# Kernel tuning notes

Measured on AMD Instinct MI355X. Metric: run time of the kernel, lower is better.

The kernel has to match this reference:

```python
import jax, jax.numpy as jnp
import numpy as np

N = 100_000      # total nodes in batched graph
E = 1_600_000    # directed edges (avg degree 16)
G = 64           # graphs in batch
F_IN = 64        # num_features
H = 64           # hl1
GF = 32          # num_global_feats
GH = 32          # global_hl1 (hard-coded in module)


def setup_inputs() -> dict:
    key = jax.random.key(0)
    ks = jax.random.split(key, 24)
    s = 0.1  # weight scale
    inp = {
        "x": jax.random.normal(ks[0], (N, F_IN), jnp.float32),
        "global_feats": jax.random.normal(ks[1], (G * GF,), jnp.float32),
        "conv0_w": jax.random.normal(ks[2], (F_IN, H), jnp.float32) * s,
        "conv0_b": jax.random.normal(ks[3], (H,), jnp.float32) * s,
        "conv1_w": jax.random.normal(ks[4], (H, H), jnp.float32) * s,
        "conv1_b": jax.random.normal(ks[5], (H,), jnp.float32) * s,
        "conv2_w": jax.random.normal(ks[6], (H, H), jnp.float32) * s,
        "conv2_b": jax.random.normal(ks[7], (H,), jnp.float32) * s,
        "lin1_w": jax.random.normal(ks[8], (H, H), jnp.float32) * s,
        "lin1_b": jax.random.normal(ks[9], (H,), jnp.float32) * s,
        "glob_w": jax.random.normal(ks[10], (GF, GH), jnp.float32) * s,
        "glob_b": jax.random.normal(ks[11], (GH,), jnp.float32) * s,
        "lin2_w": jax.random.normal(ks[12], (H + GH, H), jnp.float32) * s,
        "lin2_b": jax.random.normal(ks[13], (H,), jnp.float32) * s,
        "lin3_w": jax.random.normal(ks[14], (H, H), jnp.float32) * s,
        "lin3_b": jax.random.normal(ks[15], (H,), jnp.float32) * s,
        "lin4_w": jax.random.normal(ks[16], (H, 1), jnp.float32) * s,
        "lin4_b": jax.random.normal(ks[17], (1,), jnp.float32) * s,
        "edge_index": jax.random.randint(ks[18], (2, E), 0, N, jnp.int64) if jax.config.jax_enable_x64 else jax.random.randint(ks[18], (2, E), 0, N, jnp.int32),
        "node_graph_ids": jnp.sort(jax.random.randint(ks[19], (N,), 0, G, jnp.int32)),
    }
    return inp


def reference(x, global_feats, conv0_w, conv0_b, conv1_w, conv1_b, conv2_w, conv2_b,
              lin1_w, lin1_b, glob_w, glob_b, lin2_w, lin2_b, lin3_w, lin3_b,
              lin4_w, lin4_b, edge_index, node_graph_ids):
    # --- GCN symmetric normalization with self-loops (PyG GCNConv default) ---
    loops = jnp.arange(N, dtype=edge_index.dtype)
    src = jnp.concatenate([edge_index[0], loops])  # [E+N]
    dst = jnp.concatenate([edge_index[1], loops])
    deg = jax.ops.segment_sum(jnp.ones_like(dst, jnp.float32), dst, num_segments=N)
    dis = jax.lax.rsqrt(deg)  # deg >= 1 thanks to self-loops
    norm = (dis[src] * dis[dst])[:, None]  # [E+N, 1]

    def gcn_conv(h, W, b):
        h = h @ W                                    # [N, H]
        msg = h[src] * norm                          # gather + scale  [E+N, H]
        return jax.ops.segment_sum(msg, dst, num_segments=N) + b  # scatter-add

    h = jax.nn.relu(gcn_conv(x, conv0_w, conv0_b))
    h = jax.nn.relu(gcn_conv(h, conv1_w, conv1_b))
    h = jax.nn.relu(gcn_conv(h, conv2_w, conv2_b))

    # --- per-graph sum pooling (contiguous slices == segment_sum on sorted ids) ---
    pooled = jax.ops.segment_sum(h, node_graph_ids, num_segments=G)  # [G, H]

    gx = jax.nn.relu(global_feats.reshape(G, GF) @ glob_w + glob_b)  # [G, GH]

    z = jax.nn.relu(pooled @ lin1_w + lin1_b)
    z = jnp.concatenate([z, gx], axis=1)             # [G, H+GH]
    z = jax.nn.relu(z @ lin2_w + lin2_b)
    z = jax.nn.relu(z @ lin3_w + lin3_b)
    out = (z @ lin4_w + lin4_b).squeeze(1)           # [G]
    return out
```

## Files before the change

kernel.cpp:

```cpp
#include <hip/hip_runtime.h>
#include <hip/hip_bf16.h>

#define NTHREADS 256
#define CAP 6144
#define P1_EDGES 8192

typedef unsigned int uint32;

__device__ __forceinline__ void fma8(float4& A0, float4& A1, uint4 v, float w) {
    A0.x += __uint_as_float(v.x << 16) * w;
    A0.y += __uint_as_float(v.x & 0xffff0000u) * w;
    A0.z += __uint_as_float(v.y << 16) * w;
    A0.w += __uint_as_float(v.y & 0xffff0000u) * w;
    A1.x += __uint_as_float(v.z << 16) * w;
    A1.y += __uint_as_float(v.z & 0xffff0000u) * w;
    A1.z += __uint_as_float(v.w << 16) * w;
    A1.w += __uint_as_float(v.w & 0xffff0000u) * w;
}
__device__ __forceinline__ void acc8(float4& A0, float4& A1, uint4 v) {
    A0.x += __uint_as_float(v.x << 16);
    A0.y += __uint_as_float(v.x & 0xffff0000u);
    A0.z += __uint_as_float(v.y << 16);
    A0.w += __uint_as_float(v.y & 0xffff0000u);
    A1.x += __uint_as_float(v.z << 16);
    A1.y += __uint_as_float(v.z & 0xffff0000u);
    A1.z += __uint_as_float(v.w << 16);
    A1.w += __uint_as_float(v.w & 0xffff0000u);
}

__device__ __forceinline__ void stage_W(const float* __restrict__ W, uint32* sWp) {
    int t = threadIdx.x;
#pragma unroll
    for (int i = 0; i < 8; i++) {
        int idx = t + NTHREADS * i;
        int p = idx >> 6, c = idx & 63;
        ushort lo = __bfloat16_as_ushort(__float2bfloat16(W[(2 * p) * 64 + c]));
        ushort hi = __bfloat16_as_ushort(__float2bfloat16(W[(2 * p + 1) * 64 + c]));
        sWp[idx] = (uint32)lo | ((uint32)hi << 16);
    }
}

__device__ __forceinline__ void gemm_compute(
    const uint32* __restrict__ sWp, const float* __restrict__ sX,
    const float* __restrict__ sD, __hip_bfloat16* __restrict__ out,
    int n_rows, int row_base) {
    int t = threadIdx.x;
    int c = t & 63;
    int r0 = t >> 6;
    float acc[16];
#pragma unroll
    for (int j = 0; j < 16; j++) acc[j] = 0.f;

    for (int k = 0; k < 64; k += 4) {
        uint32 u01 = sWp[((k >> 1) + 0) * 64 + c];
        uint32 u23 = sWp[((k >> 1) + 1) * 64 + c];
        float w0 = __uint_as_float(u01 << 16);
        float w1 = __uint_as_float(u01 & 0xffff0000u);
        float w2 = __uint_as_float(u23 << 16);
        float w3 = __uint_as_float(u23 & 0xffff0000u);
#pragma unroll
        for (int j = 0; j < 16; j++) {
            float4 xv = *(const float4*)(sX + (r0 + 4 * j) * 64 + k);
            acc[j] += xv.x * w0 + xv.y * w1 + xv.z * w2 + xv.w * w3;
        }
    }

#pragma unroll
    for (int j = 0; j < 16; j++) {
        int r = row_base + r0 + 4 * j;
        if (r < n_rows) {
            float s = sD ? sD[r0 + 4 * j] : 1.0f;
            out[(size_t)r * 64 + c] = __float2bfloat16(s * acc[j]);
        }
    }
}

__global__ __launch_bounds__(NTHREADS) void pass1_gemm0(
    const int* __restrict__ ei, int nE, int* gcur, uint32* __restrict__ pbuf, int npart,
    const float* __restrict__ x, __hip_bfloat16* __restrict__ U,
    const float* __restrict__ W, int n_rows, int nP1) {
    __shared__ __align__(16) uint32 sWp[32 * 64];
    __shared__ __align__(16) float sX[64 * 64];

    int bid = blockIdx.x;
    int t = threadIdx.x;

    if (bid < nP1) {
        int* hist = (int*)sX;
        int* base = hist + npart;
        int* cnt  = base + npart;
        for (int i = t; i < npart; i += NTHREADS) { hist[i] = 0; cnt[i] = 0; }
        __syncthreads();

        int e0 = bid * P1_EDGES;
#pragma unroll 4
        for (int j = 0; j < P1_EDGES / NTHREADS; j++) {
            int e = e0 + j * NTHREADS + t;
            if (e < nE) atomicAdd(&hist[ei[nE + e] >> 8], 1);
        }
        __syncthreads();
        for (int i = t; i < npart; i += NTHREADS) {
            base[i] = hist[i] ? atomicAdd(&gcur[i * 16], hist[i]) : 0;
        }
        __syncthreads();
#pragma unroll 4
        for (int j = 0; j < P1_EDGES / NTHREADS; j++) {
            int e = e0 + j * NTHREADS + t;
            if (e < nE) {
                int s = ei[e];
                int d = ei[nE + e];
                int p = d >> 8;
                int off = atomicAdd(&cnt[p], 1);
                int pos = base[p] + off;
                if (pos < CAP) pbuf[(size_t)p * CAP + pos] = ((uint32)s << 8) | (uint32)(d & 255);
            }
        }
        return;
    }

    int row_base = (bid - nP1) * 64;
    stage_W(W, sWp);
    float4* sX4 = (float4*)sX;
#pragma unroll
    for (int i = 0; i < 4; i++) {
        int idx = t + NTHREADS * i;
        int r = row_base + (idx >> 4);
        float4 v = make_float4(0.f, 0.f, 0.f, 0.f);
        if (r < n_rows) v = ((const float4*)(x + (size_t)r * 64))[idx & 15];
        sX4[idx] = v;
    }
    __syncthreads();
    gemm_compute(sWp, sX, nullptr, U, n_rows, row_base);
}

__global__ __launch_bounds__(512) void scanP(const int* __restrict__ gcur, int* pbase,
                                             int npart, int n, int nE, int* row_ptr) {
    __shared__ int sm[512];
    int t = threadIdx.x;
    int v = (t < npart) ? gcur[t * 16] : 0;
    sm[t] = v;
    __syncthreads();
    for (int off = 1; off < 512; off <<= 1) {
        int a = (t >= off) ? sm[t - off] : 0;
        __syncthreads();
        sm[t] += a;
        __syncthreads();
    }
    if (t < npart) pbase[t] = sm[t] - v;
    if (t == 0) row_ptr[n] = nE;
}

__global__ __launch_bounds__(NTHREADS) void pass2(
    const uint32* __restrict__ pbuf, const int* __restrict__ gcur,
    const int* __restrict__ pbase, int* __restrict__ row_ptr,
    float* __restrict__ dis, int* __restrict__ col, int n) {
    __shared__ int hist[256];
    __shared__ int excl[256];
    __shared__ int cnt[256];
    __shared__ int sm[256];

    int p = blockIdx.x;
    int t = threadIdx.x;
    hist[t] = 0;
    cnt[t] = 0;
    __syncthreads();

    int total = gcur[p * 16];
    if (total > CAP) total = CAP;
    const uint32* pb = pbuf + (size_t)p * CAP;

    for (int i = t; i < total; i += NTHREADS) atomicAdd(&hist[pb[i] & 255], 1);
    __syncthreads();

    sm[t] = hist[t];
    __syncthreads();
    for (int off = 1; off < 256; off <<= 1) {
        int a = (t >= off) ? sm[t - off] : 0;
        __syncthreads();
        sm[t] += a;
        __syncthreads();
    }
    excl[t] = sm[t] - hist[t];
    __syncthreads();

    int rbase = pbase[p];
    int node = p * 256 + t;
    if (node < n) {
        row_ptr[node] = rbase + excl[t];
        dis[node] = rsqrtf(1.0f + (float)hist[t]);
    }

    for (int i = t; i < total; i += NTHREADS) {
        uint32 v = pb[i];
        int dl = v & 255;
        int off = atomicAdd(&cnt[dl], 1);
        col[rbase + excl[dl] + off] = (int)(v >> 8);
    }
}

template <bool WEIGHTED>
__device__ __forceinline__ void gather_row(
    const uint4* __restrict__ T8, const float* __restrict__ dis,
    const float* __restrict__ bias,
    const int* __restrict__ row_ptr, const int* __restrict__ col,
    int node, int q, float* __restrict__ sXrow, int n) {
    float4 o0, o1;
    if (node < n) {
        float dn = dis[node];
        float4 a0 = make_float4(0.f, 0.f, 0.f, 0.f);
        float4 a1 = make_float4(0.f, 0.f, 0.f, 0.f);
        {
            uint4 sv = T8[(size_t)node * 8 + q];
            if (WEIGHTED) fma8(a0, a1, sv, dn);
            else          acc8(a0, a1, sv);
        }
        int e0 = row_ptr[node];
        int e1 = row_ptr[node + 1];
        int e = e0;
        for (; e + 7 < e1; e += 8) {
            int s0 = col[e],     s1 = col[e + 1], s2 = col[e + 2], s3 = col[e + 3];
            int s4 = col[e + 4], s5 = col[e + 5], s6 = col[e + 6], s7 = col[e + 7];
            uint4 v0 = T8[(size_t)s0 * 8 + q];
            uint4 v1 = T8[(size_t)s1 * 8 + q];
            uint4 v2 = T8[(size_t)s2 * 8 + q];
            uint4 v3 = T8[(size_t)s3 * 8 + q];
            uint4 v4 = T8[(size_t)s4 * 8 + q];
            uint4 v5 = T8[(size_t)s5 * 8 + q];
            uint4 v6 = T8[(size_t)s6 * 8 + q];
            uint4 v7 = T8[(size_t)s7 * 8 + q];
            if (WEIGHTED) {
                fma8(a0, a1, v0, dis[s0]); fma8(a0, a1, v1, dis[s1]);
                fma8(a0, a1, v2, dis[s2]); fma8(a0, a1, v3, dis[s3]);
                fma8(a0, a1, v4, dis[s4]); fma8(a0, a1, v5, dis[s5]);
                fma8(a0, a1, v6, dis[s6]); fma8(a0, a1, v7, dis[s7]);
            } else {
                acc8(a0, a1, v0); acc8(a0, a1, v1); acc8(a0, a1, v2); acc8(a0, a1, v3);
                acc8(a0, a1, v4); acc8(a0, a1, v5); acc8(a0, a1, v6); acc8(a0, a1, v7);
            }
        }
        for (; e + 3 < e1; e += 4) {
            int s0 = col[e], s1 = col[e + 1], s2 = col[e + 2], s3 = col[e + 3];
            uint4 v0 = T8[(size_t)s0 * 8 + q];
            uint4 v1 = T8[(size_t)s1 * 8 + q];
            uint4 v2 = T8[(size_t)s2 * 8 + q];
            uint4 v3 = T8[(size_t)s3 * 8 + q];
            if (WEIGHTED) {
                fma8(a0, a1, v0, dis[s0]); fma8(a0, a1, v1, dis[s1]);
                fma8(a0, a1, v2, dis[s2]); fma8(a0, a1, v3, dis[s3]);
            } else {
                acc8(a0, a1, v0); acc8(a0, a1, v1); acc8(a0, a1, v2); acc8(a0, a1, v3);
            }
        }
        for (; e < e1; e++) {
            int s0 = col[e];
            uint4 v0 = T8[(size_t)s0 * 8 + q];
            if (WEIGHTED) fma8(a0, a1, v0, dis[s0]);
            else          acc8(a0, a1, v0);
        }
        float4 b0 = ((const float4*)bias)[q * 2];
        float4 b1 = ((const float4*)bias)[q * 2 + 1];
        o0.x = fmaxf(b0.x + dn * a0.x, 0.f);
        o0.y = fmaxf(b0.y + dn * a0.y, 0.f);
        o0.z = fmaxf(b0.z + dn * a0.z, 0.f);
        o0.w = fmaxf(b0.w + dn * a0.w, 0.f);
        o1.x = fmaxf(b1.x + dn * a1.x, 0.f);
        o1.y = fmaxf(b1.y + dn * a1.y, 0.f);
        o1.z = fmaxf(b1.z + dn * a1.z, 0.f);
        o1.w = fmaxf(b1.w + dn * a1.w, 0.f);
    } else {
        o0 = make_float4(0.f, 0.f, 0.f, 0.f);
        o1 = o0;
    }
    ((float4*)sXrow)[q * 2] = o0;
    ((float4*)sXrow)[q * 2 + 1] = o1;
}

template <bool WEIGHTED>
__global__ __launch_bounds__(NTHREADS) void agg_gemm(
    const __hip_bfloat16* __restrict__ Tin, __hip_bfloat16* __restrict__ Tout,
    const float* __restrict__ W, const float* __restrict__ dis,
    const float* __restrict__ bias,
    const int* __restrict__ row_ptr, const int* __restrict__ col, int n) {
    __shared__ __align__(16) uint32 sWp[32 * 64];
    __shared__ __align__(16) float sX[64 * 64];
    __shared__ float sD[64];
    int t = threadIdx.x;
    int row_base = blockIdx.x * 64;

    stage_W(W, sWp);
    if (t < 64) {
        int r = row_base + t;
        sD[t] = (r < n) ? dis[r] : 0.f;
    }

    const uint4* T8 = (const uint4*)Tin;
    int q = t & 7;
    int l = t >> 3;
    gather_row<WEIGHTED>(T8, dis, bias, row_ptr, col, row_base + l,      q, sX + l * 64,        n);
    gather_row<WEIGHTED>(T8, dis, bias, row_ptr, col, row_base + 32 + l, q, sX + (32 + l) * 64, n);
    __syncthreads();

    gemm_compute(sWp, sX, sD, Tout, n, row_base);
}

__global__ __launch_bounds__(NTHREADS) void agg_pool(
    const __hip_bfloat16* __restrict__ Tin,
    const float* __restrict__ dis, const float* __restrict__ bias,
    const int* __restrict__ row_ptr, const int* __restrict__ col,
    const int* __restrict__ gid, float* __restrict__ pooled, int n) {
    __shared__ __align__(16) float sX[64 * 64];
    __shared__ int sG[64];
    int t = threadIdx.x;
    int row_base = blockIdx.x * 64;

    if (t < 64) {
        int r = row_base + t;
        sG[t] = (r < n) ? gid[r] : -1;
    }

    const uint4* T8 = (const uint4*)Tin;
    int q = t & 7;
    int l = t >> 3;
    gather_row<false>(T8, dis, bias, row_ptr, col, row_base + l,      q, sX + l * 64,        n);
    gather_row<false>(T8, dis, bias, row_ptr, col, row_base + 32 + l, q, sX + (32 + l) * 64, n);
    __syncthreads();

    int f = t & 63;
    int w = t >> 6;
    float racc = 0.f;
    int cur = -1;
#pragma unroll
    for (int i = 0; i < 16; i++) {
        int r = i * 4 + w;
        int g = sG[r];
        if (g != cur) {
            if (cur >= 0 && racc != 0.f) atomicAdd(&pooled[cur * 64 + f], racc);
            racc = 0.f;
            cur = g;
        }
        if (g >= 0) racc += sX[r * 64 + f];
    }
    if (cur >= 0 && racc != 0.f) atomicAdd(&pooled[cur * 64 + f], racc);
}

__global__ __launch_bounds__(NTHREADS) void head_kernel(
    const float* __restrict__ pooled, const float* __restrict__ gf,
    const float* __restrict__ glob_w, const float* __restrict__ glob_b,
    const float* __restrict__ lin1_w, const float* __restrict__ lin1_b,
    const float* __restrict__ lin2_w, const float* __restrict__ lin2_b,
    const float* __restrict__ lin3_w, const float* __restrict__ lin3_b,
    const float* __restrict__ lin4_w, const float* __restrict__ lin4_b,
    float* __restrict__ out) {
    __shared__ float gx[64 * 32];
    __shared__ float zA[64 * 64];
    __shared__ float zB[64 * 64];
    int t = threadIdx.x;

    for (int i = t; i < 64 * 32; i += NTHREADS) {
        int g = i >> 5, j = i & 31;
        float acc = glob_b[j];
        for (int k = 0; k < 32; k++) acc += gf[g * 32 + k] * glob_w[k * 32 + j];
        gx[i] = fmaxf(acc, 0.f);
    }
    for (int i = t; i < 4096; i += NTHREADS) {
        int g = i >> 6, j = i & 63;
        float acc = lin1_b[j];
        for (int k = 0; k < 64; k++) acc += pooled[g * 64 + k] * lin1_w[k * 64 + j];
        zA[i] = fmaxf(acc, 0.f);
    }
    __syncthreads();
    for (int i = t; i < 4096; i += NTHREADS) {
        int g = i >> 6, j = i & 63;
        float acc = lin2_b[j];
        for (int k = 0; k < 64; k++) acc += zA[g * 64 + k] * lin2_w[k * 64 + j];
        for (int k = 0; k < 32; k++) acc += gx[g * 32 + k] * lin2_w[(64 + k) * 64 + j];
        zB[i] = fmaxf(acc, 0.f);
    }
    __syncthreads();
    for (int i = t; i < 4096; i += NTHREADS) {
        int g = i >> 6, j = i & 63;
        float acc = lin3_b[j];
        for (int k = 0; k < 64; k++) acc += zB[g * 64 + k] * lin3_w[k * 64 + j];
        zA[i] = fmaxf(acc, 0.f);
    }
    __syncthreads();
    if (t < 64) {
        float acc = lin4_b[0];
        for (int k = 0; k < 64; k++) acc += zA[t * 64 + k] * lin4_w[k];
        out[t] = acc;
    }
}

extern "C" void kernel_launch(void* const* d_in, const int* in_sizes, int n_in,
                              void* d_out, int out_size, void* d_ws, size_t ws_size,
                              hipStream_t stream) {
    const float* x      = (const float*)d_in[0];
    const float* gf     = (const float*)d_in[1];
    const float* conv_w[3] = {(const float*)d_in[2], (const float*)d_in[4], (const float*)d_in[6]};
    const float* conv_b[3] = {(const float*)d_in[3], (const float*)d_in[5], (const float*)d_in[7]};
    const float* lin1_w = (const float*)d_in[8];
    const float* lin1_b = (const float*)d_in[9];
    const float* glob_w = (const float*)d_in[10];
    const float* glob_b = (const float*)d_in[11];
    const float* lin2_w = (const float*)d_in[12];
    const float* lin2_b = (const float*)d_in[13];
    const float* lin3_w = (const float*)d_in[14];
    const float* lin3_b = (const float*)d_in[15];
    const float* lin4_w = (const float*)d_in[16];
    const float* lin4_b = (const float*)d_in[17];
    const int* ei  = (const int*)d_in[18];
    const int* gid = (const int*)d_in[19];

    const int N = in_sizes[0] / 64;
    const int E = in_sizes[18] / 2;
    const int NPART = (N + 255) >> 8;

    char* ws = (char*)d_ws;
    float* dis     = (float*)ws;                 ws += (size_t)N * 4;
    float* pooled  = (float*)ws;                 ws += 4096 * 4;
    __hip_bfloat16* U  = (__hip_bfloat16*)ws;    ws += (size_t)N * 64 * 2;
    __hip_bfloat16* T1 = (__hip_bfloat16*)ws;    ws += (size_t)N * 64 * 2;
    int*   row_ptr = (int*)ws;                   ws += ((size_t)N + 4) * 4;
    int*   col     = (int*)ws;                   ws += (size_t)E * 4;
    uint32* pbuf   = (uint32*)ws;                ws += (size_t)NPART * CAP * 4;
    int*   gcur    = (int*)ws;                   ws += (size_t)NPART * 16 * 4;
    int*   pbase   = (int*)ws;                   ws += (size_t)((NPART + 15) & ~15) * 4;

    const int nP1 = (E + P1_EDGES - 1) / P1_EDGES;
    const int gemm_blocks = (N + 63) / 64;

    hipMemsetAsync(gcur, 0, (size_t)NPART * 16 * 4, stream);
    hipMemsetAsync(pooled, 0, 4096 * 4, stream);
    pass1_gemm0<<<nP1 + gemm_blocks, NTHREADS, 0, stream>>>(
        ei, E, gcur, pbuf, NPART, x, U, conv_w[0], N, nP1);

    scanP<<<1, 512, 0, stream>>>(gcur, pbase, NPART, N, E, row_ptr);
    pass2<<<NPART, NTHREADS, 0, stream>>>(pbuf, gcur, pbase, row_ptr, dis, col, N);

    agg_gemm<true><<<gemm_blocks, NTHREADS, 0, stream>>>(
        U, T1, conv_w[1], dis, conv_b[0], row_ptr, col, N);

    agg_gemm<false><<<gemm_blocks, NTHREADS, 0, stream>>>(
        T1, U, conv_w[2], dis, conv_b[1], row_ptr, col, N);

    agg_pool<<<gemm_blocks, NTHREADS, 0, stream>>>(
        U, dis, conv_b[2], row_ptr, col, gid, pooled, N);

    head_kernel<<<1, NTHREADS, 0, stream>>>(pooled, gf,
                                            glob_w, glob_b, lin1_w, lin1_b,
                                            lin2_w, lin2_b, lin3_w, lin3_b,
                                            lin4_w, lin4_b, (float*)d_out);
}
```

Measured before the change: 254.7 us.

## Split bf16 feature tables into two 32-column planes for gather locality

Node feature tables are stored as two separate planes of 32 bf16 columns each instead of one 64-column row. Gathers read one plane for all edges, then the other, with 4 threads per row instead of 8, so each plane's working set is half the size and may stay in cache better. The weights are also kept in shared memory as fp32 instead of packed bf16, which removes the unpacking in the GEMM inner loop but doubles the LDS footprint. The trade-off is reading the col/dis indices twice per node and a different occupancy profile.

Measured after the change: 281.2 us. 10.4% more time.

```diff
diff --git a/kernel.cpp b/kernel.cpp
--- a/kernel.cpp
+++ b/kernel.cpp
@@ -28,21 +28,18 @@
     A1.w += __uint_as_float(v.w & 0xffff0000u);
 }
 
-__device__ __forceinline__ void stage_W(const float* __restrict__ W, uint32* sWp) {
-    int t = threadIdx.x;
-#pragma unroll
-    for (int i = 0; i < 8; i++) {
-        int idx = t + NTHREADS * i;
-        int p = idx >> 6, c = idx & 63;
-        ushort lo = __bfloat16_as_ushort(__float2bfloat16(W[(2 * p) * 64 + c]));
-        ushort hi = __bfloat16_as_ushort(__float2bfloat16(W[(2 * p + 1) * 64 + c]));
-        sWp[idx] = (uint32)lo | ((uint32)hi << 16);
-    }
+__device__ __forceinline__ void stage_W(const float* __restrict__ W, float* sW) {
+    int t = threadIdx.x;
+    const float4* W4 = (const float4*)W;
+    float4* sW4 = (float4*)sW;
+#pragma unroll
+    for (int i = 0; i < 4; i++) sW4[t + NTHREADS * i] = W4[t + NTHREADS * i];
 }
 
 __device__ __forceinline__ void gemm_compute(
-    const uint32* __restrict__ sWp, const float* __restrict__ sX,
-    const float* __restrict__ sD, __hip_bfloat16* __restrict__ out,
+    const float* __restrict__ sW, const float* __restrict__ sX,
+    const float* __restrict__ sD,
+    __hip_bfloat16* __restrict__ out_lo, __hip_bfloat16* __restrict__ out_hi,
     int n_rows, int row_base) {
     int t = threadIdx.x;
     int c = t & 63;
@@ -52,12 +49,10 @@
     for (int j = 0; j < 16; j++) acc[j] = 0.f;
 
     for (int k = 0; k < 64; k += 4) {
-        uint32 u01 = sWp[((k >> 1) + 0) * 64 + c];
-        uint32 u23 = sWp[((k >> 1) + 1) * 64 + c];
-        float w0 = __uint_as_float(u01 << 16);
-        float w1 = __uint_as_float(u01 & 0xffff0000u);
-        float w2 = __uint_as_float(u23 << 16);
-        float w3 = __uint_as_float(u23 & 0xffff0000u);
+        float w0 = sW[(k + 0) * 64 + c];
+        float w1 = sW[(k + 1) * 64 + c];
+        float w2 = sW[(k + 2) * 64 + c];
+        float w3 = sW[(k + 3) * 64 + c];
 #pragma unroll
         for (int j = 0; j < 16; j++) {
             float4 xv = *(const float4*)(sX + (r0 + 4 * j) * 64 + k);
@@ -65,21 +60,24 @@
         }
     }
 
+    __hip_bfloat16* outp = (c < 32) ? out_lo : out_hi;
+    int cl = c & 31;
 #pragma unroll
     for (int j = 0; j < 16; j++) {
         int r = row_base + r0 + 4 * j;
         if (r < n_rows) {
             float s = sD ? sD[r0 + 4 * j] : 1.0f;
-            out[(size_t)r * 64 + c] = __float2bfloat16(s * acc[j]);
+            outp[(size_t)r * 32 + cl] = __float2bfloat16(s * acc[j]);
         }
     }
 }
 
 __global__ __launch_bounds__(NTHREADS) void pass1_gemm0(
     const int* __restrict__ ei, int nE, int* gcur, uint32* __restrict__ pbuf, int npart,
-    const float* __restrict__ x, __hip_bfloat16* __restrict__ U,
+    const float* __restrict__ x,
+    __hip_bfloat16* __restrict__ U_lo, __hip_bfloat16* __restrict__ U_hi,
     const float* __restrict__ W, int n_rows, int nP1) {
-    __shared__ __align__(16) uint32 sWp[32 * 64];
+    __shared__ __align__(16) float sW[64 * 64];
     __shared__ __align__(16) float sX[64 * 64];
 
     int bid = blockIdx.x;
@@ -119,7 +117,7 @@
     }
 
     int row_base = (bid - nP1) * 64;
-    stage_W(W, sWp);
+    stage_W(W, sW);
     float4* sX4 = (float4*)sX;
 #pragma unroll
     for (int i = 0; i < 4; i++) {
@@ -130,7 +128,7 @@
         sX4[idx] = v;
     }
     __syncthreads();
-    gemm_compute(sWp, sX, nullptr, U, n_rows, row_base);
+    gemm_compute(sW, sX, nullptr, U_lo, U_hi, n_rows, row_base);
 }
 
 __global__ __launch_bounds__(512) void scanP(const int* __restrict__ gcur, int* pbase,
@@ -199,9 +197,9 @@
 }
 
 template <bool WEIGHTED>
-__device__ __forceinline__ void gather_row(
-    const uint4* __restrict__ T8, const float* __restrict__ dis,
-    const float* __restrict__ bias,
+__device__ __forceinline__ void gather_plane(
+    const uint4* __restrict__ P, const float* __restrict__ dis,
+    const float* __restrict__ biasp,
     const int* __restrict__ row_ptr, const int* __restrict__ col,
     int node, int q, float* __restrict__ sXrow, int n) {
     float4 o0, o1;
@@ -210,7 +208,7 @@
         float4 a0 = make_float4(0.f, 0.f, 0.f, 0.f);
         float4 a1 = make_float4(0.f, 0.f, 0.f, 0.f);
         {
-            uint4 sv = T8[(size_t)node * 8 + q];
+            uint4 sv = P[(size_t)node * 4 + q];
             if (WEIGHTED) fma8(a0, a1, sv, dn);
             else          acc8(a0, a1, sv);
         }
@@ -220,14 +218,14 @@
         for (; e + 7 < e1; e += 8) {
             int s0 = col[e],     s1 = col[e + 1], s2 = col[e + 2], s3 = col[e + 3];
             int s4 = col[e + 4], s5 = col[e + 5], s6 = col[e + 6], s7 = col[e + 7];
-            uint4 v0 = T8[(size_t)s0 * 8 + q];
-            uint4 v1 = T8[(size_t)s1 * 8 + q];
-            uint4 v2 = T8[(size_t)s2 * 8 + q];
-            uint4 v3 = T8[(size_t)s3 * 8 + q];
-            uint4 v4 = T8[(size_t)s4 * 8 + q];
-            uint4 v5 = T8[(size_t)s5 * 8 + q];
-            uint4 v6 = T8[(size_t)s6 * 8 + q];
-            uint4 v7 = T8[(size_t)s7 * 8 + q];
+            uint4 v0 = P[(size_t)s0 * 4 + q];
+            uint4 v1 = P[(size_t)s1 * 4 + q];
+            uint4 v2 = P[(size_t)s2 * 4 + q];
+            uint4 v3 = P[(size_t)s3 * 4 + q];
+            uint4 v4 = P[(size_t)s4 * 4 + q];
+            uint4 v5 = P[(size_t)s5 * 4 + q];
+            uint4 v6 = P[(size_t)s6 * 4 + q];
+            uint4 v7 = P[(size_t)s7 * 4 + q];
             if (WEIGHTED) {
                 fma8(a0, a1, v0, dis[s0]); fma8(a0, a1, v1, dis[s1]);
                 fma8(a0, a1, v2, dis[s2]); fma8(a0, a1, v3, dis[s3]);
@@ -240,10 +238,10 @@
         }
         for (; e + 3 < e1; e += 4) {
             int s0 = col[e], s1 = col[e + 1], s2 = col[e + 2], s3 = col[e + 3];
-            uint4 v0 = T8[(size_t)s0 * 8 + q];
-            uint4 v1 = T8[(size_t)s1 * 8 + q];
-            uint4 v2 = T8[(size_t)s2 * 8 + q];
-            uint4 v3 = T8[(size_t)s3 * 8 + q];
+            uint4 v0 = P[(size_t)s0 * 4 + q];
+            uint4 v1 = P[(size_t)s1 * 4 + q];
+            uint4 v2 = P[(size_t)s2 * 4 + q];
+            uint4 v3 = P[(size_t)s3 * 4 + q];
             if (WEIGHTED) {
                 fma8(a0, a1, v0, dis[s0]); fma8(a0, a1, v1, dis[s1]);
                 fma8(a0, a1, v2, dis[s2]); fma8(a0, a1, v3, dis[s3]);
@@ -253,12 +251,12 @@
         }
         for (; e < e1; e++) {
             int s0 = col[e];
-            uint4 v0 = T8[(size_t)s0 * 8 + q];
+            uint4 v0 = P[(size_t)s0 * 4 + q];
             if (WEIGHTED) fma8(a0, a1, v0, dis[s0]);
             else          acc8(a0, a1, v0);
         }
-        float4 b0 = ((const float4*)bias)[q * 2];
-        float4 b1 = ((const float4*)bias)[q * 2 + 1];
+        float4 b0 = ((const float4*)biasp)[q * 2];
+        float4 b1 = ((const float4*)biasp)[q * 2 + 1];
         o0.x = fmaxf(b0.x + dn * a0.x, 0.f);
         o0.y = fmaxf(b0.y + dn * a0.y, 0.f);
         o0.z = fmaxf(b0.z + dn * a0.z, 0.f);
@@ -277,34 +275,36 @@
 
 template <bool WEIGHTED>
 __global__ __launch_bounds__(NTHREADS) void agg_gemm(
-    const __hip_bfloat16* __restrict__ Tin, __hip_bfloat16* __restrict__ Tout,
+    const __hip_bfloat16* __restrict__ Tin_lo, const __hip_bfloat16* __restrict__ Tin_hi,
+    __hip_bfloat16* __restrict__ Tout_lo, __hip_bfloat16* __restrict__ Tout_hi,
     const float* __restrict__ W, const float* __restrict__ dis,
     const float* __restrict__ bias,
     const int* __restrict__ row_ptr, const int* __restrict__ col, int n) {
-    __shared__ __align__(16) uint32 sWp[32 * 64];
+    __shared__ __align__(16) float sW[64 * 64];
     __shared__ __align__(16) float sX[64 * 64];
     __shared__ float sD[64];
     int t = threadIdx.x;
     int row_base = blockIdx.x * 64;
 
-    stage_W(W, sWp);
+    stage_W(W, sW);
     if (t < 64) {
         int r = row_base + t;
         sD[t] = (r < n) ? dis[r] : 0.f;
     }
 
-    const uint4* T8 = (const uint4*)Tin;
-    int q = t & 7;
-    int l = t >> 3;
-    gather_row<WEIGHTED>(T8, dis, bias, row_ptr, col, row_base + l,      q, sX + l * 64,        n);
-    gather_row<WEIGHTED>(T8, dis, bias, row_ptr, col, row_base + 32 + l, q, sX + (32 + l) * 64, n);
-    __syncthreads();
-
-    gemm_compute(sWp, sX, sD, Tout, n, row_base);
+    int q = t & 3;
+    int l = t >> 2;
+    gather_plane<WEIGHTED>((const uint4*)Tin_lo, dis, bias,      row_ptr, col,
+                           row_base + l, q, sX + l * 64,      n);
+    gather_plane<WEIGHTED>((const uint4*)Tin_hi, dis, bias + 32, row_ptr, col,
+                           row_base + l, q, sX + l * 64 + 32, n);
+    __syncthreads();
+
+    gemm_compute(sW, sX, sD, Tout_lo, Tout_hi, n, row_base);
 }
 
 __global__ __launch_bounds__(NTHREADS) void agg_pool(
-    const __hip_bfloat16* __restrict__ Tin,
+    const __hip_bfloat16* __restrict__ Tin_lo, const __hip_bfloat16* __restrict__ Tin_hi,
     const float* __restrict__ dis, const float* __restrict__ bias,
     const int* __restrict__ row_ptr, const int* __restrict__ col,
     const int* __restrict__ gid, float* __restrict__ pooled, int n) {
@@ -318,11 +318,12 @@
         sG[t] = (r < n) ? gid[r] : -1;
     }
 
-    const uint4* T8 = (const uint4*)Tin;
-    int q = t & 7;
-    int l = t >> 3;
-    gather_row<false>(T8, dis, bias, row_ptr, col, row_base + l,      q, sX + l * 64,        n);
-    gather_row<false>(T8, dis, bias, row_ptr, col, row_base + 32 + l, q, sX + (32 + l) * 64, n);
+    int q = t & 3;
+    int l = t >> 2;
+    gather_plane<false>((const uint4*)Tin_lo, dis, bias,      row_ptr, col,
+                        row_base + l, q, sX + l * 64,      n);
+    gather_plane<false>((const uint4*)Tin_hi, dis, bias + 32, row_ptr, col,
+                        row_base + l, q, sX + l * 64 + 32, n);
     __syncthreads();
 
     int f = t & 63;
@@ -418,8 +419,10 @@
     char* ws = (char*)d_ws;
     float* dis     = (float*)ws;                 ws += (size_t)N * 4;
     float* pooled  = (float*)ws;                 ws += 4096 * 4;
-    __hip_bfloat16* U  = (__hip_bfloat16*)ws;    ws += (size_t)N * 64 * 2;
-    __hip_bfloat16* T1 = (__hip_bfloat16*)ws;    ws += (size_t)N * 64 * 2;
+    __hip_bfloat16* U_lo  = (__hip_bfloat16*)ws; ws += (size_t)N * 32 * 2;
+    __hip_bfloat16* U_hi  = (__hip_bfloat16*)ws; ws += (size_t)N * 32 * 2;
+    __hip_bfloat16* T1_lo = (__hip_bfloat16*)ws; ws += (size_t)N * 32 * 2;
+    __hip_bfloat16* T1_hi = (__hip_bfloat16*)ws; ws += (size_t)N * 32 * 2;
     int*   row_ptr = (int*)ws;                   ws += ((size_t)N + 4) * 4;
     int*   col     = (int*)ws;                   ws += (size_t)E * 4;
     uint32* pbuf   = (uint32*)ws;                ws += (size_t)NPART * CAP * 4;
@@ -432,19 +435,19 @@
     hipMemsetAsync(gcur, 0, (size_t)NPART * 16 * 4, stream);
     hipMemsetAsync(pooled, 0, 4096 * 4, stream);
     pass1_gemm0<<<nP1 + gemm_blocks, NTHREADS, 0, stream>>>(
-        ei, E, gcur, pbuf, NPART, x, U, conv_w[0], N, nP1);
+        ei, E, gcur, pbuf, NPART, x, U_lo, U_hi, conv_w[0], N, nP1);
 
     scanP<<<1, 512, 0, stream>>>(gcur, pbase, NPART, N, E, row_ptr);
     pass2<<<NPART, NTHREADS, 0, stream>>>(pbuf, gcur, pbase, row_ptr, dis, col, N);
 
     agg_gemm<true><<<gemm_blocks, NTHREADS, 0, stream>>>(
-        U, T1, conv_w[1], dis, conv_b[0], row_ptr, col, N);
+        U_lo, U_hi, T1_lo, T1_hi, conv_w[1], dis, conv_b[0], row_ptr, col, N);
 
     agg_gemm<false><<<gemm_blocks, NTHREADS, 0, stream>>>(
-        T1, U, conv_w[2], dis, conv_b[1], row_ptr, col, N);
+        T1_lo, T1_hi, U_lo, U_hi, conv_w[2], dis, conv_b[1], row_ptr, col, N);
 
     agg_pool<<<gemm_blocks, NTHREADS, 0, stream>>>(
-        U, dis, conv_b[2], row_ptr, col, gid, pooled, N);
+        U_lo, U_hi, dis, conv_b[2], row_ptr, col, gid, pooled, N);
 
     head_kernel<<<1, NTHREADS, 0, stream>>>(pooled, gf,
                                             glob_w, glob_b, lin1_w, lin1_b,
```
